# Kernel tuning notes

Measured on AMD Instinct MI355X. Metric: run time of the kernel, lower is better.

The kernel has to match this reference:

```python
import jax, jax.numpy as jnp
from jax import lax
import numpy as np

BETA = 0.5       # leak factor of snn.Leaky
THR = 1.0        # firing threshold
SLOPE = 25.0     # fast_sigmoid surrogate slope (snntorch default)
NUM_STEPS = 16

@jax.custom_vjp
def spike(m):
    # Heaviside of (mem - threshold); surrogate grad = 1/(slope*|m|+1)^2
    return (m > 0).astype(m.dtype)

def _spike_fwd(m):
    return spike(m), m

def _spike_bwd(m, g):
    return (g / (SLOPE * jnp.abs(m) + 1.0) ** 2,)

spike.defvjp(_spike_fwd, _spike_bwd)


def setup_inputs() -> dict:
    key = jax.random.key(0)
    k1, k2, k3 = jax.random.split(key, 3)
    x = jax.random.uniform(k1, (4096, 1, 28, 28), dtype=jnp.float32)
    conv_w = jax.random.normal(k2, (8, 1, 3, 3), dtype=jnp.float32) * 0.3
    fc_w = jax.random.normal(k3, (10, 1352), dtype=jnp.float32) * 0.05
    return {"x": x, "conv_w": conv_w, "fc_w": fc_w}


def reference(x, conv_w, fc_w):
    B = x.shape[0]
    # conv1(x) is identical every timestep -> compute once (same math).
    cur1 = lax.conv_general_dilated(
        x, conv_w, window_strides=(1, 1), padding='VALID',
        dimension_numbers=('NCHW', 'OIHW', 'NCHW'))  # [B,8,26,26]

    mem1_0 = jnp.zeros_like(cur1)
    mem2_0 = jnp.zeros((B, 10), dtype=x.dtype)

    def step(carry, _):
        mem1, mem2 = carry
        # LIF layer 1: integrate, fire, subtract-reset (reset detached)
        mem1 = BETA * mem1 + cur1
        spk1 = spike(mem1 - THR)
        mem1 = mem1 - lax.stop_gradient(spk1) * THR
        # avg pool 2x2 -> [B,8,13,13]
        pool = spk1.reshape(B, 8, 13, 2, 13, 2).mean(axis=(3, 5))
        # fc (no bias): [B,1352] @ [1352,10]
        cur2 = pool.reshape(B, -1) @ fc_w.T
        # LIF layer 2
        mem2 = BETA * mem2 + cur2
        spk2 = spike(mem2 - THR)
        mem2 = mem2 - lax.stop_gradient(spk2) * THR
        return (mem1, mem2), spk2

    (_, _), spk2_rec = lax.scan(step, (mem1_0, mem2_0), None, length=NUM_STEPS)
    return spk2_rec.sum(axis=0)  # [B,10] spike counts
```

## Files before the change

kernel.cpp:

```cpp
#include <hip/hip_runtime.h>


typedef float v2f __attribute__((ext_vector_type(2)));
typedef float f32x4 __attribute__((ext_vector_type(4)));
typedef short s16x8 __attribute__((ext_vector_type(8)));

#if __has_builtin(__builtin_elementwise_fma)
#define VFMA(a, b, c) __builtin_elementwise_fma((a), (b), (c))
#else
#define VFMA(a, b, c) ((a) * (b) + (c))
#endif

#define NU 6
#define KS 43
#define SPLITS 4

__device__ __forceinline__ unsigned short bf16_rne(float f) {
    unsigned u = __float_as_uint(f);
    return (unsigned short)((u + 0x7FFFu + ((u >> 16) & 1u)) >> 16);
}
__device__ __forceinline__ float bf16_back(unsigned short h) {
    return __uint_as_float(((unsigned)h) << 16);
}

__device__ __forceinline__ unsigned bf16pair(float flo, float fhi) {
#if __has_builtin(__builtin_amdgcn_perm)
    return __builtin_amdgcn_perm(__float_as_uint(fhi), __float_as_uint(flo),
                                 0x07060302u);
#else
    return (__float_as_uint(fhi) & 0xFFFF0000u) | (__float_as_uint(flo) >> 16);
#endif
}

__global__ void build_bfrag_kernel(const float* __restrict__ fc_w,
                                   s16x8* __restrict__ wsfrag) {
    const int blk = blockIdx.x;
    const int p   = blk / KS;
    const int ks  = blk - p * KS;
    const int l   = threadIdx.x;
    s16x8 frag;
    #pragma unroll
    for (int jj = 0; jj < 8; ++jj) {
        const int k = ks * 32 + (l >> 4) * 8 + jj;
        const int n = l & 15;
        float r = (k < 1352 && n < 10) ? 0.25f * fc_w[n * 1352 + k] : 0.0f;
        unsigned short b = 0;
        for (int q = 0; q <= p; ++q) {
            b = bf16_rne(r);
            r -= bf16_back(b);
        }
        frag[jj] = (short)b;
    }
    wsfrag[blk * 64 + l] = frag;
}

__global__ __launch_bounds__(256, 4) void snn_fused_kernel(
    const float* __restrict__ x,
    const float* __restrict__ conv_w,
    const s16x8* __restrict__ wsfrag,
    float* __restrict__ out)
{
    const int b    = blockIdx.x;
    const int tid  = threadIdx.x;
    const int lane = tid & 63;
    const int wid  = tid >> 6;

    __shared__ __align__(16) unsigned char sAb[KS * 544];
    __shared__ float scC[4 * 256];
    __shared__ float scw[72];
    __shared__ float scur2[160];

    if (tid < 72) scw[tid] = conv_w[tid];

    int xbase[NU], kbase[NU], sbase[NU];
    #pragma unroll
    for (int i = 0; i < NU; ++i) {
        const int u      = tid + 256 * i;
        const bool valid = (u < 1352);
        const int uu  = valid ? u : 0;
        const int k   = uu / 169;
        const int rem = uu - k * 169;
        const int pr  = rem / 13;
        const int pc  = rem - pr * 13;
        xbase[i] = 56 * pr + 2 * pc;
        kbase[i] = 9 * k;
        const int uo = u & 31;
        sbase[i] = (u >> 5) * 544 + (uo >> 3) * 136 + (uo & 7);
    }
    __syncthreads();

    const float* xb = x + (size_t)b * 784;
    v2f cur2[NU][2];
    v2f mem2[NU][2];
    #pragma unroll
    for (int i = 0; i < NU; ++i) {
        float cw[9];
        #pragma unroll
        for (int qq = 0; qq < 9; ++qq) cw[qq] = scw[kbase[i] + qq];

        float xr[4][4];
        #pragma unroll
        for (int r = 0; r < 4; ++r) {
            const float2* rp = reinterpret_cast<const float2*>(xb + xbase[i] + 28 * r);
            const float2 a = rp[0], c2 = rp[1];
            xr[r][0] = a.x; xr[r][1] = a.y; xr[r][2] = c2.x; xr[r][3] = c2.y;
        }

        const bool valid = (tid + 256 * i) < 1352;
        float cell[2][2];
        #pragma unroll
        for (int dr = 0; dr < 2; ++dr)
            #pragma unroll
            for (int dc = 0; dc < 2; ++dc) {
                float acc = 0.0f;
                #pragma unroll
                for (int ki = 0; ki < 3; ++ki)
                    #pragma unroll
                    for (int kj = 0; kj < 3; ++kj)
                        acc += xr[dr + ki][dc + kj] * cw[ki * 3 + kj];
                cell[dr][dc] = valid ? acc : 0.0f;
            }
        cur2[i][0] = (v2f){cell[0][0], cell[0][1]};
        cur2[i][1] = (v2f){cell[1][0], cell[1][1]};
        mem2[i][0] = (v2f){0.0f, 0.0f};
        mem2[i][1] = (v2f){0.0f, 0.0f};
    }

    const v2f half2 = (v2f){0.5f, 0.5f};

    #pragma unroll
    for (int t = 0; t < 16; ++t) {
        #pragma unroll
        for (int i = 0; i < NU; ++i) {
            v2f m01 = VFMA(half2, mem2[i][0], cur2[i][0]);
            v2f m23 = VFMA(half2, mem2[i][1], cur2[i][1]);
            v2f sp01, sp23;
            sp01.x = m01.x > 1.0f ? 1.0f : 0.0f;
            sp01.y = m01.y > 1.0f ? 1.0f : 0.0f;
            sp23.x = m23.x > 1.0f ? 1.0f : 0.0f;
            sp23.y = m23.y > 1.0f ? 1.0f : 0.0f;
            mem2[i][0] = m01 - sp01;
            mem2[i][1] = m23 - sp23;
            v2f s = sp01 + sp23;
            const float c = s.x + s.y;
            if (i < 5 || tid < 96)
                sAb[sbase[i] + t * 8] = (unsigned char)(unsigned)c;
        }
    }
    __syncthreads();

    {
        const int p = wid;
        f32x4 acc = (f32x4){0.f, 0.f, 0.f, 0.f};
        const int arow = (lane >> 4) * 136 + (lane & 15) * 8;
        #pragma unroll 2
        for (int ks = 0; ks < KS; ++ks) {
            const uint2 av = *reinterpret_cast<const uint2*>(&sAb[ks * 544 + arow]);
            const float f0 = (float)( av.x        & 0xFF);
            const float f1 = (float)((av.x >>  8) & 0xFF);
            const float f2 = (float)((av.x >> 16) & 0xFF);
            const float f3 = (float)( av.x >> 24);
            const float f4 = (float)( av.y        & 0xFF);
            const float f5 = (float)((av.y >>  8) & 0xFF);
            const float f6 = (float)((av.y >> 16) & 0xFF);
            const float f7 = (float)( av.y >> 24);
            union { uint4 u; s16x8 v; } au;
            au.u.x = bf16pair(f0, f1);
            au.u.y = bf16pair(f2, f3);
            au.u.z = bf16pair(f4, f5);
            au.u.w = bf16pair(f6, f7);

            const s16x8 bw = wsfrag[(p * KS + ks) * 64 + lane];
            acc = __builtin_amdgcn_mfma_f32_16x16x32_bf16(au.v, bw, acc, 0, 0, 0);
        }
        const int o = lane & 15;
        #pragma unroll
        for (int r = 0; r < 4; ++r) {
            const int t = (lane >> 4) * 4 + r;
            scC[wid * 256 + t * 16 + o] = acc[r];
        }
    }
    __syncthreads();

    if (tid < 160) {
        const int t = tid / 10;
        const int o = tid - t * 10;
        const int idx = t * 16 + o;
        scur2[tid] = (scC[idx] + scC[256 + idx]) + (scC[512 + idx] + scC[768 + idx]);
    }
    __syncthreads();

    if (tid < 10) {
        float m2 = 0.0f, cnt = 0.0f;
        #pragma unroll
        for (int t = 0; t < 16; ++t) {
            m2 = __builtin_fmaf(0.5f, m2, scur2[t * 10 + tid]);
            float ms = m2 - 1.0f;
            bool  sp = ms > 0.0f;
            m2  = sp ? ms : m2;
            cnt += sp ? 1.0f : 0.0f;
        }
        out[(size_t)b * 10 + tid] = cnt;
    }
}

extern "C" void kernel_launch(void* const* d_in, const int* in_sizes, int n_in,
                              void* d_out, int out_size, void* d_ws, size_t ws_size,
                              hipStream_t stream) {
    const float* x      = (const float*)d_in[0];
    const float* conv_w = (const float*)d_in[1];
    const float* fc_w   = (const float*)d_in[2];
    float* out          = (float*)d_out;
    s16x8* wsfrag       = (s16x8*)d_ws;

    build_bfrag_kernel<<<SPLITS * KS, 64, 0, stream>>>(fc_w, wsfrag);

    const int B = in_sizes[0] / 784;
    snn_fused_kernel<<<B, 256, 0, stream>>>(x, conv_w, wsfrag, out);
}
```

Before: 78.88 us.

## Process two images per block to reuse fc weight fragments across MFMAs

```diff
diff --git a/kernel.cpp b/kernel.cpp
--- a/kernel.cpp
+++ b/kernel.cpp
@@ -14,6 +14,8 @@
 #define NU 6
 #define KS 43
 #define SPLITS 4
+#define IMG 2
+#define SA_BYTES (KS * 544)
 
 __device__ __forceinline__ unsigned short bf16_rne(float f) {
     unsigned u = __float_as_uint(f);
@@ -30,6 +32,23 @@
 #else
     return (__float_as_uint(fhi) & 0xFFFF0000u) | (__float_as_uint(flo) >> 16);
 #endif
+}
+
+__device__ __forceinline__ s16x8 unpack8(uint2 av) {
+    const float f0 = (float)( av.x        & 0xFF);
+    const float f1 = (float)((av.x >>  8) & 0xFF);
+    const float f2 = (float)((av.x >> 16) & 0xFF);
+    const float f3 = (float)( av.x >> 24);
+    const float f4 = (float)( av.y        & 0xFF);
+    const float f5 = (float)((av.y >>  8) & 0xFF);
+    const float f6 = (float)((av.y >> 16) & 0xFF);
+    const float f7 = (float)( av.y >> 24);
+    union { uint4 u; s16x8 v; } au;
+    au.u.x = bf16pair(f0, f1);
+    au.u.y = bf16pair(f2, f3);
+    au.u.z = bf16pair(f4, f5);
+    au.u.w = bf16pair(f6, f7);
+    return au.v;
 }
 
 __global__ void build_bfrag_kernel(const float* __restrict__ fc_w,
@@ -54,25 +73,26 @@
     wsfrag[blk * 64 + l] = frag;
 }
 
-__global__ __launch_bounds__(256, 4) void snn_fused_kernel(
+__global__ __launch_bounds__(256, 3) void snn_fused_kernel(
     const float* __restrict__ x,
     const float* __restrict__ conv_w,
     const s16x8* __restrict__ wsfrag,
     float* __restrict__ out)
 {
-    const int b    = blockIdx.x;
+    const int b0   = blockIdx.x * IMG;
     const int tid  = threadIdx.x;
     const int lane = tid & 63;
     const int wid  = tid >> 6;
 
-    __shared__ __align__(16) unsigned char sAb[KS * 544];
-    __shared__ float scC[4 * 256];
+    __shared__ __align__(16) unsigned char sAb[IMG * SA_BYTES];
+    __shared__ float scur2[IMG * 160];
     __shared__ float scw[72];
-    __shared__ float scur2[160];
+    float* const scC = reinterpret_cast<float*>(sAb);
 
     if (tid < 72) scw[tid] = conv_w[tid];
 
     int xbase[NU], kbase[NU], sbase[NU];
+    bool uvalid[NU];
     #pragma unroll
     for (int i = 0; i < NU; ++i) {
         const int u      = tid + 256 * i;
@@ -82,48 +102,51 @@
         const int rem = uu - k * 169;
         const int pr  = rem / 13;
         const int pc  = rem - pr * 13;
-        xbase[i] = 56 * pr + 2 * pc;
-        kbase[i] = 9 * k;
+        xbase[i]  = 56 * pr + 2 * pc;
+        kbase[i]  = 9 * k;
+        uvalid[i] = valid;
         const int uo = u & 31;
         sbase[i] = (u >> 5) * 544 + (uo >> 3) * 136 + (uo & 7);
     }
     __syncthreads();
 
-    const float* xb = x + (size_t)b * 784;
-    v2f cur2[NU][2];
-    v2f mem2[NU][2];
-    #pragma unroll
-    for (int i = 0; i < NU; ++i) {
-        float cw[9];
+    v2f cur2[IMG][NU][2];
+    v2f mem2[IMG][NU][2];
+    #pragma unroll
+    for (int img = 0; img < IMG; ++img) {
+        const float* xb = x + (size_t)(b0 + img) * 784;
         #pragma unroll
-        for (int qq = 0; qq < 9; ++qq) cw[qq] = scw[kbase[i] + qq];
-
-        float xr[4][4];
-        #pragma unroll
-        for (int r = 0; r < 4; ++r) {
-            const float2* rp = reinterpret_cast<const float2*>(xb + xbase[i] + 28 * r);
-            const float2 a = rp[0], c2 = rp[1];
-            xr[r][0] = a.x; xr[r][1] = a.y; xr[r][2] = c2.x; xr[r][3] = c2.y;
-        }
-
-        const bool valid = (tid + 256 * i) < 1352;
-        float cell[2][2];
-        #pragma unroll
-        for (int dr = 0; dr < 2; ++dr)
-            #pragma unroll
-            for (int dc = 0; dc < 2; ++dc) {
-                float acc = 0.0f;
+        for (int i = 0; i < NU; ++i) {
+            float cw[9];
+            #pragma unroll
+            for (int qq = 0; qq < 9; ++qq) cw[qq] = scw[kbase[i] + qq];
+
+            float xr[4][4];
+            #pragma unroll
+            for (int r = 0; r < 4; ++r) {
+                const float2* rp = reinterpret_cast<const float2*>(xb + xbase[i] + 28 * r);
+                const float2 a = rp[0], c2 = rp[1];
+                xr[r][0] = a.x; xr[r][1] = a.y; xr[r][2] = c2.x; xr[r][3] = c2.y;
+            }
+
+            float cell[2][2];
+            #pragma unroll
+            for (int dr = 0; dr < 2; ++dr)
                 #pragma unroll
-                for (int ki = 0; ki < 3; ++ki)
+                for (int dc = 0; dc < 2; ++dc) {
+                    float acc = 0.0f;
                     #pragma unroll
-                    for (int kj = 0; kj < 3; ++kj)
-                        acc += xr[dr + ki][dc + kj] * cw[ki * 3 + kj];
-                cell[dr][dc] = valid ? acc : 0.0f;
-            }
-        cur2[i][0] = (v2f){cell[0][0], cell[0][1]};
-        cur2[i][1] = (v2f){cell[1][0], cell[1][1]};
-        mem2[i][0] = (v2f){0.0f, 0.0f};
-        mem2[i][1] = (v2f){0.0f, 0.0f};
+                    for (int ki = 0; ki < 3; ++ki)
+                        #pragma unroll
+                        for (int kj = 0; kj < 3; ++kj)
+                            acc += xr[dr + ki][dc + kj] * cw[ki * 3 + kj];
+                    cell[dr][dc] = uvalid[i] ? acc : 0.0f;
+                }
+            cur2[img][i][0] = (v2f){cell[0][0], cell[0][1]};
+            cur2[img][i][1] = (v2f){cell[1][0], cell[1][1]};
+            mem2[img][i][0] = (v2f){0.0f, 0.0f};
+            mem2[img][i][1] = (v2f){0.0f, 0.0f};
+        }
     }
 
     const v2f half2 = (v2f){0.5f, 0.5f};
@@ -131,76 +154,75 @@
     #pragma unroll
     for (int t = 0; t < 16; ++t) {
         #pragma unroll
-        for (int i = 0; i < NU; ++i) {
-            v2f m01 = VFMA(half2, mem2[i][0], cur2[i][0]);
-            v2f m23 = VFMA(half2, mem2[i][1], cur2[i][1]);
-            v2f sp01, sp23;
-            sp01.x = m01.x > 1.0f ? 1.0f : 0.0f;
-            sp01.y = m01.y > 1.0f ? 1.0f : 0.0f;
-            sp23.x = m23.x > 1.0f ? 1.0f : 0.0f;
-            sp23.y = m23.y > 1.0f ? 1.0f : 0.0f;
-            mem2[i][0] = m01 - sp01;
-            mem2[i][1] = m23 - sp23;
-            v2f s = sp01 + sp23;
-            const float c = s.x + s.y;
-            if (i < 5 || tid < 96)
-                sAb[sbase[i] + t * 8] = (unsigned char)(unsigned)c;
-        }
-    }
-    __syncthreads();
-
+        for (int img = 0; img < IMG; ++img) {
+            #pragma unroll
+            for (int i = 0; i < NU; ++i) {
+                v2f m01 = VFMA(half2, mem2[img][i][0], cur2[img][i][0]);
+                v2f m23 = VFMA(half2, mem2[img][i][1], cur2[img][i][1]);
+                v2f sp01, sp23;
+                sp01.x = m01.x > 1.0f ? 1.0f : 0.0f;
+                sp01.y = m01.y > 1.0f ? 1.0f : 0.0f;
+                sp23.x = m23.x > 1.0f ? 1.0f : 0.0f;
+                sp23.y = m23.y > 1.0f ? 1.0f : 0.0f;
+                mem2[img][i][0] = m01 - sp01;
+                mem2[img][i][1] = m23 - sp23;
+                v2f s = sp01 + sp23;
+                const float c = s.x + s.y;
+                if (i < 5 || tid < 96)
+                    sAb[img * SA_BYTES + sbase[i] + t * 8] =
+                        (unsigned char)(unsigned)c;
+            }
+        }
+    }
+    __syncthreads();
+
+    f32x4 acc0 = (f32x4){0.f, 0.f, 0.f, 0.f};
+    f32x4 acc1 = (f32x4){0.f, 0.f, 0.f, 0.f};
     {
         const int p = wid;
-        f32x4 acc = (f32x4){0.f, 0.f, 0.f, 0.f};
         const int arow = (lane >> 4) * 136 + (lane & 15) * 8;
         #pragma unroll 2
         for (int ks = 0; ks < KS; ++ks) {
-            const uint2 av = *reinterpret_cast<const uint2*>(&sAb[ks * 544 + arow]);
-            const float f0 = (float)( av.x        & 0xFF);
-            const float f1 = (float)((av.x >>  8) & 0xFF);
-            const float f2 = (float)((av.x >> 16) & 0xFF);
-            const float f3 = (float)( av.x >> 24);
-            const float f4 = (float)( av.y        & 0xFF);
-            const float f5 = (float)((av.y >>  8) & 0xFF);
-            const float f6 = (float)((av.y >> 16) & 0xFF);
-            const float f7 = (float)( av.y >> 24);
-            union { uint4 u; s16x8 v; } au;
-            au.u.x = bf16pair(f0, f1);
-            au.u.y = bf16pair(f2, f3);
-            au.u.z = bf16pair(f4, f5);
-            au.u.w = bf16pair(f6, f7);
-
+            const uint2 a0 = *reinterpret_cast<const uint2*>(&sAb[ks * 544 + arow]);
+            const uint2 a1 = *reinterpret_cast<const uint2*>(&sAb[SA_BYTES + ks * 544 + arow]);
             const s16x8 bw = wsfrag[(p * KS + ks) * 64 + lane];
-            acc = __builtin_amdgcn_mfma_f32_16x16x32_bf16(au.v, bw, acc, 0, 0, 0);
-        }
+            acc0 = __builtin_amdgcn_mfma_f32_16x16x32_bf16(unpack8(a0), bw, acc0, 0, 0, 0);
+            acc1 = __builtin_amdgcn_mfma_f32_16x16x32_bf16(unpack8(a1), bw, acc1, 0, 0, 0);
+        }
+    }
+    __syncthreads();
+
+    {
         const int o = lane & 15;
-        #pragma unroll
-        for (int r = 0; r < 4; ++r) {
-            const int t = (lane >> 4) * 4 + r;
-            scC[wid * 256 + t * 16 + o] = acc[r];
-        }
-    }
-    __syncthreads();
-
-    if (tid < 160) {
-        const int t = tid / 10;
-        const int o = tid - t * 10;
-        const int idx = t * 16 + o;
-        scur2[tid] = (scC[idx] + scC[256 + idx]) + (scC[512 + idx] + scC[768 + idx]);
-    }
-    __syncthreads();
-
-    if (tid < 10) {
+        if (o < 10) {
+            #pragma unroll
+            for (int r = 0; r < 4; ++r) {
+                const int t = (lane >> 4) * 4 + r;
+                scC[wid * 320 +       t * 10 + o] = acc0[r];
+                scC[wid * 320 + 160 + t * 10 + o] = acc1[r];
+            }
+        }
+    }
+    __syncthreads();
+
+    for (int idx = tid; idx < IMG * 160; idx += 256) {
+        scur2[idx] = (scC[idx] + scC[320 + idx]) + (scC[640 + idx] + scC[960 + idx]);
+    }
+    __syncthreads();
+
+    if (tid < 20) {
+        const int img = tid / 10;
+        const int o   = tid - img * 10;
         float m2 = 0.0f, cnt = 0.0f;
         #pragma unroll
         for (int t = 0; t < 16; ++t) {
-            m2 = __builtin_fmaf(0.5f, m2, scur2[t * 10 + tid]);
+            m2 = __builtin_fmaf(0.5f, m2, scur2[img * 160 + t * 10 + o]);
             float ms = m2 - 1.0f;
             bool  sp = ms > 0.0f;
             m2  = sp ? ms : m2;
             cnt += sp ? 1.0f : 0.0f;
         }
-        out[(size_t)b * 10 + tid] = cnt;
+        out[(size_t)(b0 + img) * 10 + o] = cnt;
     }
 }
 
@@ -216,5 +238,5 @@
     build_bfrag_kernel<<<SPLITS * KS, 64, 0, stream>>>(fc_w, wsfrag);
 
     const int B = in_sizes[0] / 784;
-    snn_fused_kernel<<<B, 256, 0, stream>>>(x, conv_w, wsfrag, out);
-}
+    snn_fused_kernel<<<B / IMG, 256, 0, stream>>>(x, conv_w, wsfrag, out);
+}
```

Measured after the change: 175.4 us. 2.22x slower.
